# Optimization experiments

Measured on AMD Instinct MI355X. Metric: run time of the kernel, lower is better.

## Reference

```python
import jax, jax.numpy as jnp
import numpy as np

N_NODES = 100000
N_EDGES = 3200000
G_EDGES = 1600000
D_FEAT = 256
K_CLUSTERS = 16
COLLAPSE_REG = 0.1


def setup_inputs() -> dict:
    key = jax.random.key(0)
    ks = jax.random.split(key, 12)
    inp = {
        'features': jax.random.normal(ks[0], (N_NODES, D_FEAT), dtype=jnp.float32),
        'W': jax.random.normal(ks[1], (D_FEAT, K_CLUSTERS), dtype=jnp.float32) / np.sqrt(D_FEAT),
        'b': jnp.zeros((K_CLUSTERS,), dtype=jnp.float32),
        'adj_src': jax.random.randint(ks[2], (N_EDGES,), 0, N_NODES, dtype=jnp.int32),
        'adj_dst': jax.random.randint(ks[3], (N_EDGES,), 0, N_NODES, dtype=jnp.int32),
        'adj_val': jax.random.uniform(ks[4], (N_EDGES,), dtype=jnp.float32),
        'g1_src': jax.random.randint(ks[5], (G_EDGES,), 0, N_NODES, dtype=jnp.int32),
        'g1_dst': jax.random.randint(ks[6], (G_EDGES,), 0, N_NODES, dtype=jnp.int32),
        'g1_val': jax.random.uniform(ks[7], (G_EDGES,), dtype=jnp.float32),
        'g2_src': jax.random.randint(ks[8], (G_EDGES,), 0, N_NODES, dtype=jnp.int32),
        'g2_dst': jax.random.randint(ks[9], (G_EDGES,), 0, N_NODES, dtype=jnp.int32),
        'g2_val': jax.random.uniform(ks[10], (G_EDGES,), dtype=jnp.float32),
        'lamda': 1,
    }
    return inp


def _spmm(src, dst, val, X, n):
    # (sparse A) @ X where A[src, dst] = val : out[i] = sum_j A[i,j] X[j]
    return jax.ops.segment_sum(val[:, None] * X[dst], src, num_segments=n)


def _col_degrees(src, dst, val, n):
    # tf.sparse.reduce_sum(A, axis=0): column sums
    return jax.ops.segment_sum(val, dst, num_segments=n)


def reference(features, W, b, adj_src, adj_dst, adj_val,
              g1_src, g1_dst, g1_val, g2_src, g2_dst, g2_val, lamda):
    n = features.shape[0]
    k = W.shape[1]
    # soft cluster assignments  [n, k]
    S = jax.nn.softmax(features @ W + b, axis=1)
    cluster_sizes = jnp.sum(S, axis=0)            # [k]
    S_pool = S / cluster_sizes                    # [n, k]

    # full-graph modularity
    deg = _col_degrees(adj_src, adj_dst, adj_val, n)  # [n]
    m = jnp.sum(deg)                                  # total edge weight
    AS = _spmm(adj_src, adj_dst, adj_val, S, n)       # [n, k]
    graph_pooled = AS.T @ S                           # [k, k]
    dS = deg @ S                                      # [k] = S^T deg
    normalizer = jnp.outer(dS, dS) / 2.0 / m          # [k, k]
    spectral_loss = -jnp.trace(graph_pooled - normalizer) / 2.0 / m

    # per-group modularity Q_g
    def group_Q(src, dst, val):
        gdeg = _col_degrees(src, dst, val, n)
        gm = jnp.sum(gdeg)
        safe_gm = jnp.where(gm > 0, gm, 1.0)
        gAS = _spmm(src, dst, val, S, n)
        g_pooled = gAS.T @ S
        gdS = gdeg @ S
        g_norm = jnp.outer(gdS, gdS) / 2.0 / safe_gm
        Qg = jnp.trace(g_pooled - g_norm) / 2.0 / m
        return jnp.where(gm > 0, Qg, 0.0), gm

    Q1, m1 = group_Q(g1_src, g1_dst, g1_val)
    Q2, m2 = group_Q(g2_src, g2_dst, g2_val)
    Q_min = jnp.minimum(Q1, Q2)
    g_edges_mean = (m1 + m2) / 2.0
    edge_ratio = m / (g_edges_mean + 1e-8)
    fairness_loss = edge_ratio * (-Q_min)

    collapse_loss = (jnp.linalg.norm(cluster_sizes) / n) * jnp.sqrt(jnp.float32(k)) - 1.0

    total_loss = spectral_loss + lamda * fairness_loss + COLLAPSE_REG * collapse_loss

    features_pooled = jax.nn.selu(S_pool.T @ features)  # [k, d]
    return features_pooled, S, total_loss
```

## Files before the change

### kernel.cpp

```cpp
#include <hip/hip_runtime.h>
#include <cstddef>
#include <cstdint>


#define G1_MAX   1024
#define EGRID    2048
#define NSEG     16
#define OFF_E    0
#define SZ_E     (3 * 18 * EGRID)
#define OFF_R    (OFF_E + SZ_E)
#define OFF_G    (OFF_R + 4112)
#define OFF_F8   (OFF_G + 64)

#define TROWS    32
#define RPAD2    134

#define BLK0     1024
#define BLK12    512

typedef int      iv4 __attribute__((ext_vector_type(4)));
typedef float    fv4 __attribute__((ext_vector_type(4)));
typedef _Float16 hh;
typedef hh       h2  __attribute__((ext_vector_type(2)));

#if __has_builtin(__builtin_amdgcn_cvt_pk_f32_fp8)
#define HW_FP8 1
#endif

__device__ __forceinline__ h2 bch2(unsigned u) { return __builtin_bit_cast(h2, u); }

__device__ __forceinline__ float fdot2(h2 a, h2 b, float c)
{
#if __has_builtin(__builtin_amdgcn_fdot2)
    return __builtin_amdgcn_fdot2(a, b, c, false);
#else
    return fmaf((float)a[0], (float)b[0], fmaf((float)a[1], (float)b[1], c));
#endif
}

__device__ __forceinline__ h2 pk16(float x, float y)
{
#if __has_builtin(__builtin_amdgcn_cvt_pkrtz)
    return __builtin_bit_cast(h2, __builtin_amdgcn_cvt_pkrtz(x, y));
#else
    h2 r; r[0] = (hh)x; r[1] = (hh)y; return r;
#endif
}

__device__ __forceinline__ unsigned f32_to_e4m3(float f)
{
    unsigned bits = __float_as_uint(f);
    unsigned s = bits >> 31;
    int e32 = (int)((bits >> 23) & 255);
    unsigned m23 = bits & 0x7FFFFF;
    int e = e32 - 120;
    unsigned out;
    if (e32 == 0) out = 0;
    else if (e <= 0) {
        float av = fabsf(f);
        int q = (int)(av * 512.0f + 0.5f);
        out = (unsigned)q;
    } else if (e > 15) out = (15u << 3) | 6u;
    else {
        unsigned m3 = (m23 + 0x80000u) >> 20;
        if (m3 == 8u) { m3 = 0u; ++e; if (e > 15) { e = 15; m3 = 6u; } }
        out = ((unsigned)e << 3) | m3;
    }
    return out | (s << 7);
}

__device__ __forceinline__ void decode16(uint4 r, float* o, const float* lut)
{
#ifdef HW_FP8
    #pragma unroll
    for (int j = 0; j < 4; ++j) {
        unsigned u = (&r.x)[j];
        auto lo = __builtin_amdgcn_cvt_pk_f32_fp8(u, false);
        auto hi = __builtin_amdgcn_cvt_pk_f32_fp8(u, true);
        o[4*j]   = lo[0]; o[4*j+1] = lo[1];
        o[4*j+2] = hi[0]; o[4*j+3] = hi[1];
    }
#else
    #pragma unroll
    for (int j = 0; j < 4; ++j) {
        unsigned u = (&r.x)[j];
        #pragma unroll
        for (int q = 0; q < 4; ++q)
            o[4*j+q] = lut[(u >> (8*q)) & 255];
    }
#endif
}

__global__ void __launch_bounds__(256)
k_rows(const float* __restrict__ F, const float* __restrict__ W,
       const float* __restrict__ b, float* __restrict__ S_out,
       unsigned* __restrict__ S_f8, float* __restrict__ ws_P, int n, int n_tiles)
{
    __shared__ h2    Wt_h2[16][RPAD2];
    __shared__ h2    rows_h2[TROWS][RPAD2];
    __shared__ float S_lds[TROWS][17];
    __shared__ float cs_red[256];

    const int t = threadIdx.x;

    for (int idx = t; idx < 2048; idx += 256) {
        int k = idx & 15, p = idx >> 4;
        Wt_h2[k][p] = pk16(W[(2*p) * 16 + k], W[(2*p + 1) * 16 + k]);
    }

    const float bk = b[t & 15];
    const int rl = t >> 4;
    const int kl = t & 15;
    const int kp = t & 15;
    const int cp = t >> 4;

    h2 Pa[8];
    #pragma unroll
    for (int j = 0; j < 8; ++j) Pa[j] = pk16(0.f, 0.f);
    float cs_acc = 0.f;

    float4 stg[8];
    auto load_tile = [&](int tl) {
        const float4* F4 = (const float4*)(F + (size_t)tl * TROWS * 256);
        #pragma unroll
        for (int q = 0; q < 8; ++q) {
            int idx = t + (q << 8);
            int r = idx >> 6;
            float4 z = {0.f, 0.f, 0.f, 0.f};
            stg[q] = (tl * TROWS + r < n) ? F4[idx] : z;
        }
    };
    if (blockIdx.x < (unsigned)n_tiles) load_tile(blockIdx.x);
    __syncthreads();

    for (int tile = blockIdx.x; tile < n_tiles; tile += gridDim.x) {
        #pragma unroll
        for (int q = 0; q < 8; ++q) {
            int idx = t + (q << 8);
            int r = idx >> 6, c4 = idx & 63;
            rows_h2[r][c4 * 2]     = pk16(stg[q].x, stg[q].y);
            rows_h2[r][c4 * 2 + 1] = pk16(stg[q].z, stg[q].w);
        }
        __syncthreads();

        {
            int nt2 = tile + gridDim.x;
            if (nt2 < n_tiles) load_tile(nt2);
        }

        float a0 = 0.f, a1 = 0.f;
        #pragma unroll 8
        for (int dd = 0; dd < 32; ++dd) {
            uint4 wv = *(const uint4*)&Wt_h2[kl][dd << 2];
            uint4 r0 = *(const uint4*)&rows_h2[rl][dd << 2];
            uint4 r1 = *(const uint4*)&rows_h2[rl + 16][dd << 2];
            #pragma unroll
            for (int j = 0; j < 4; ++j) {
                h2 wj = bch2((&wv.x)[j]);
                a0 = fdot2(wj, bch2((&r0.x)[j]), a0);
                a1 = fdot2(wj, bch2((&r1.x)[j]), a1);
            }
        }
        a0 += bk; a1 += bk;

        float mx0 = a0, mx1 = a1;
        #pragma unroll
        for (int o = 8; o; o >>= 1) {
            mx0 = fmaxf(mx0, __shfl_xor(mx0, o, 16));
            mx1 = fmaxf(mx1, __shfl_xor(mx1, o, 16));
        }
        float e0 = __expf(a0 - mx0), e1 = __expf(a1 - mx1);
        float s0 = e0, s1 = e1;
        #pragma unroll
        for (int o = 8; o; o >>= 1) {
            s0 += __shfl_xor(s0, o, 16);
            s1 += __shfl_xor(s1, o, 16);
        }
        float sv0 = e0 / s0, sv1 = e1 / s1;

        const bool v0 = (tile * TROWS + rl) < n;
        const bool v1 = (tile * TROWS + rl + 16) < n;
        if (v0) { S_out[(((size_t)(tile * TROWS + rl)) << 4) + kl] = sv0; cs_acc += sv0; }
        if (v1) { S_out[(((size_t)(tile * TROWS + rl + 16)) << 4) + kl] = sv1; cs_acc += sv1; }
        S_lds[rl][kl]      = v0 ? sv0 : 0.f;
        S_lds[rl + 16][kl] = v1 ? sv1 : 0.f;
        __syncthreads();

        if (t < 128) {
            int r = t >> 2, c = t & 3;
            int row = tile * TROWS + r;
            if (row < n) {
                unsigned u = f32_to_e4m3(S_lds[r][4*c])
                           | (f32_to_e4m3(S_lds[r][4*c+1]) << 8)
                           | (f32_to_e4m3(S_lds[r][4*c+2]) << 16)
                           | (f32_to_e4m3(S_lds[r][4*c+3]) << 24);
                S_f8[((size_t)row << 2) + c] = u;
            }
        }

        #pragma unroll 4
        for (int r = 0; r < TROWS; ++r) {
            float sv = S_lds[r][kp];
            h2 svh = pk16(sv, sv);
            uint4 fa = *(const uint4*)&rows_h2[r][cp << 3];
            uint4 fb = *(const uint4*)&rows_h2[r][(cp << 3) + 4];
            #pragma unroll
            for (int j = 0; j < 4; ++j) {
                Pa[j]     = svh * bch2((&fa.x)[j]) + Pa[j];
                Pa[4 + j] = svh * bch2((&fb.x)[j]) + Pa[4 + j];
            }
        }
        __syncthreads();
    }

    {
        float o16[16];
        #pragma unroll
        for (int j = 0; j < 8; ++j) {
            o16[2*j]     = (float)Pa[j][0];
            o16[2*j + 1] = (float)Pa[j][1];
        }
        float* dst = ws_P + (size_t)blockIdx.x * 4112 + kp * 256 + (cp << 4);
        #pragma unroll
        for (int j = 0; j < 4; ++j)
            *(float4*)&dst[4*j] = make_float4(o16[4*j], o16[4*j+1], o16[4*j+2], o16[4*j+3]);
    }
    cs_red[t] = cs_acc;
    __syncthreads();
    if (t < 16) {
        float ssum = 0.f;
        #pragma unroll
        for (int i = 0; i < 16; ++i) ssum += cs_red[t + (i << 4)];
        ws_P[(size_t)blockIdx.x * 4112 + 4096 + t] = ssum;
    }
}

__global__ void __launch_bounds__(256)
k_reduce(const float* __restrict__ ws_P, float* __restrict__ ws_red, int nb)
{
    const int seg  = blockIdx.x & (NSEG - 1);
    const int jblk = blockIdx.x / NSEG;
    const int idx  = jblk * 256 + threadIdx.x;
    if (idx >= 4112) return;
    const int chunk = (nb + NSEG - 1) / NSEG;
    const int b0 = seg * chunk;
    const int b1 = min(nb, b0 + chunk);
    float s = 0.f;
    for (int bb = b0; bb < b1; ++bb)
        s += ws_P[(size_t)bb * 4112 + idx];
    atomicAdd(&ws_red[idx], s);
}

__global__ void __launch_bounds__(256, 4)
k_edge(const int* __restrict__ src0, const int* __restrict__ dst0,
       const float* __restrict__ val0, int n0,
       const int* __restrict__ src1, const int* __restrict__ dst1,
       const float* __restrict__ val1, int n1,
       const int* __restrict__ src2, const int* __restrict__ dst2,
       const float* __restrict__ val2, int n2,
       const uint4* __restrict__ S8, float* __restrict__ ws_e,
       int b0, int b1)
{
#ifndef HW_FP8
    __shared__ float lut[256];
    if (threadIdx.x < 256) {
        int i = threadIdx.x;
        int e_ = (i >> 3) & 15, m_ = i & 7, s_ = i >> 7;
        float v = e_ ? ldexpf((float)(8 + m_), e_ - 10) : ldexpf((float)m_, -9);
        lut[i] = s_ ? -v : v;
    }
    __syncthreads();
    const float* lutp = lut;
#else
    const float* lutp = nullptr;
#endif

    int g, bb, nblk, nE;
    const int* src; const int* dst; const float* val;
    if ((int)blockIdx.x < b0)      { g = 0; bb = blockIdx.x;      nblk = b0;             src = src0; dst = dst0; val = val0; nE = n0; }
    else if ((int)blockIdx.x < b1) { g = 1; bb = blockIdx.x - b0; nblk = b1 - b0;        src = src1; dst = dst1; val = val1; nE = n1; }
    else                           { g = 2; bb = blockIdx.x - b1; nblk = gridDim.x - b1; src = src2; dst = dst2; val = val2; nE = n2; }

    float m_acc = 0.f, tr_acc = 0.f;
    float gds[16];
    #pragma unroll
    for (int k = 0; k < 16; ++k) gds[k] = 0.f;

    const int nv = nE >> 2;
    const iv4* s4 = (const iv4*)src;
    const iv4* d4 = (const iv4*)dst;
    const fv4* v4 = (const fv4*)val;
    const int stride = nblk * 256;

    for (int i = bb * 256 + threadIdx.x; i < nv; i += stride) {
        iv4 sa = __builtin_nontemporal_load(&s4[i]);
        iv4 da = __builtin_nontemporal_load(&d4[i]);
        fv4 va = __builtin_nontemporal_load(&v4[i]);
        uint4 rs[4], rd[4];
        #pragma unroll
        for (int e = 0; e < 4; ++e) {
            rs[e] = S8[sa[e]];
            rd[e] = S8[da[e]];
        }
        #pragma unroll
        for (int e = 0; e < 4; ++e) {
            float sv[16], dv[16];
            decode16(rs[e], sv, lutp);
            decode16(rd[e], dv, lutp);
            float v = va[e];
            float dot = 0.f;
            #pragma unroll
            for (int k = 0; k < 16; ++k) dot = fmaf(sv[k], dv[k], dot);
            m_acc += v;
            tr_acc = fmaf(v, dot, tr_acc);
            #pragma unroll
            for (int k = 0; k < 16; ++k) gds[k] = fmaf(v, dv[k], gds[k]);
        }
    }

    if (bb == 0) {
        int e = (nv << 2) + threadIdx.x;
        if (e < nE) {
            float sv[16], dv[16];
            decode16(S8[src[e]], sv, lutp);
            decode16(S8[dst[e]], dv, lutp);
            float v = val[e];
            float dot = 0.f;
            #pragma unroll
            for (int k = 0; k < 16; ++k) dot = fmaf(sv[k], dv[k], dot);
            m_acc += v;
            tr_acc = fmaf(v, dot, tr_acc);
            #pragma unroll
            for (int k = 0; k < 16; ++k) gds[k] = fmaf(v, dv[k], gds[k]);
        }
    }

    #pragma unroll
    for (int o = 32; o; o >>= 1) {
        m_acc  += __shfl_xor(m_acc, o);
        tr_acc += __shfl_xor(tr_acc, o);
        #pragma unroll
        for (int k = 0; k < 16; ++k) gds[k] += __shfl_xor(gds[k], o);
    }
    __shared__ float wred[4][18];
    const int wid = threadIdx.x >> 6, lane = threadIdx.x & 63;
    if (lane == 0) {
        wred[wid][0] = m_acc; wred[wid][1] = tr_acc;
        #pragma unroll
        for (int k = 0; k < 16; ++k) wred[wid][2 + k] = gds[k];
    }
    __syncthreads();
    if (threadIdx.x < 18) {
        float s = wred[0][threadIdx.x] + wred[1][threadIdx.x]
                + wred[2][threadIdx.x] + wred[3][threadIdx.x];
        ws_e[(size_t)g * 18 * EGRID + (size_t)threadIdx.x * EGRID + bb] = s;
    }
}

__global__ void __launch_bounds__(256)
k_ereduce(const float* __restrict__ ws_e, float* __restrict__ G54,
          int g0, int g1, int g2)
{
    const int p = blockIdx.x;
    const int g = p / 18, slot = p % 18;
    int grids[3] = {g0, g1, g2};
    const int gb = grids[g];
    const float* base = ws_e + (size_t)g * 18 * EGRID + (size_t)slot * EGRID;

    const int t = threadIdx.x;
    float s = 0.f;
    for (int bb = t; bb < gb; bb += 256) s += base[bb];
    #pragma unroll
    for (int o = 32; o; o >>= 1) s += __shfl_xor(s, o);

    __shared__ float wr[4];
    if ((t & 63) == 0) wr[t >> 6] = s;
    __syncthreads();
    if (t == 0) G54[p] = wr[0] + wr[1] + wr[2] + wr[3];
}

__global__ void __launch_bounds__(256)
k_final(const float* __restrict__ ws_red, const float* __restrict__ G54,
        const void* __restrict__ lamda_ptr, float* __restrict__ out, int n)
{
    __shared__ float G[54];
    const int t = threadIdx.x;
    if (t < 54) G[t] = G54[t];
    __syncthreads();

    const float* P  = ws_red;
    const float* cs = ws_red + 4096;

    const float scale = 1.0507009873554805f;
    const float alpha = 1.6732632423543772f;
    for (int idx = t; idx < 4096; idx += 256) {
        int k = idx >> 8;
        float x = P[idx] / cs[k];
        float y = x > 0.f ? scale * x : scale * alpha * (expf(x) - 1.f);
        out[idx] = y;
    }

    if (t == 0) {
        int   li = *(const int*)lamda_ptr;
        float lf = *(const float*)lamda_ptr;
        float lamda = (li > -100000 && li < 100000) ? (float)li : lf;

        float m = G[0], trA = G[1];
        float ds2 = 0.f;
        for (int k = 0; k < 16; ++k) ds2 += G[2 + k] * G[2 + k];
        float spectral = -(trA - ds2 / (2.f * m)) / (2.f * m);

        float Q[2], gm[2];
        for (int g = 0; g < 2; ++g) {
            const float* Gg = G + 18 * (g + 1);
            float mg = Gg[0], trg = Gg[1];
            float gds2 = 0.f;
            for (int k = 0; k < 16; ++k) gds2 += Gg[2 + k] * Gg[2 + k];
            float safe = mg > 0.f ? mg : 1.f;
            float q = (trg - gds2 / (2.f * safe)) / (2.f * m);
            Q[g]  = mg > 0.f ? q : 0.f;
            gm[g] = mg;
        }
        float Qmin = fminf(Q[0], Q[1]);
        float gmean = 0.5f * (gm[0] + gm[1]);
        float fairness = (m / (gmean + 1e-8f)) * (-Qmin);

        float csn = 0.f;
        for (int k = 0; k < 16; ++k) csn += cs[k] * cs[k];
        float collapse = (sqrtf(csn) / (float)n) * 4.f - 1.f;

        out[4096 + (size_t)n * 16] = spectral + lamda * fairness + 0.1f * collapse;
    }
}

extern "C" void kernel_launch(void* const* d_in, const int* in_sizes, int n_in,
                              void* d_out, int out_size, void* d_ws, size_t ws_size,
                              hipStream_t stream)
{
    const float* F       = (const float*)d_in[0];
    const float* W       = (const float*)d_in[1];
    const float* b       = (const float*)d_in[2];
    const int*   adj_src = (const int*)d_in[3];
    const int*   adj_dst = (const int*)d_in[4];
    const float* adj_val = (const float*)d_in[5];
    const int*   g1_src  = (const int*)d_in[6];
    const int*   g1_dst  = (const int*)d_in[7];
    const float* g1_val  = (const float*)d_in[8];
    const int*   g2_src  = (const int*)d_in[9];
    const int*   g2_dst  = (const int*)d_in[10];
    const float* g2_val  = (const float*)d_in[11];
    const void*  lamda_p = d_in[12];

    const int n  = in_sizes[0] / 256;
    const int nE = in_sizes[3];
    const int n1 = in_sizes[6];
    const int n2 = in_sizes[9];

    float* out   = (float*)d_out;
    float* S_out = out + 4096;

    float* ws   = (float*)d_ws;
    float* ws_e = ws + OFF_E;
    float* ws_r = ws + OFF_R;
    float* ws_g = ws + OFF_G;
    unsigned* S8 = (unsigned*)(ws + OFF_F8);
    const size_t off_p = (size_t)OFF_F8 + (size_t)n * 4;
    float* ws_P = ws + off_p;

    const int n_tiles = (n + TROWS - 1) / TROWS;
    long avail = ((long)(ws_size / 4) - (long)off_p) / 4112;
    int grid1 = n_tiles < G1_MAX ? n_tiles : G1_MAX;
    if (avail < grid1) grid1 = (int)avail;
    if (grid1 < 1) grid1 = 1;

    (void)hipMemsetAsync(ws_r, 0, 4112 * sizeof(float), stream);

    k_rows<<<grid1, 256, 0, stream>>>(F, W, b, S_out, S8, ws_P, n, n_tiles);
    k_reduce<<<17 * NSEG, 256, 0, stream>>>(ws_P, ws_r, grid1);

    const int b0 = BLK0, b1g = BLK12, b2g = BLK12;
    k_edge<<<b0 + b1g + b2g, 256, 0, stream>>>(
        adj_src, adj_dst, adj_val, nE,
        g1_src, g1_dst, g1_val, n1,
        g2_src, g2_dst, g2_val, n2,
        (const uint4*)S8, ws_e, b0, b0 + b1g);

    k_ereduce<<<54, 256, 0, stream>>>(ws_e, ws_g, b0, b1g, b2g);
    k_final<<<1, 256, 0, stream>>>(ws_r, ws_g, lamda_p, out, n);
}
```

Baseline: 153.2 us.

## Use MFMA f16 instructions for softmax logits and pooled-feature accumulation in k_rows

Replaces the scalar fdot2 logits computation and the packed-half FMA accumulation of S^T·F with 16x16x32 f16 MFMA instructions. It adds a transposed LDS copy of each feature tile and a transposed f16 copy of S, and splits the K dimension across waves with an LDS reduction. S is now written from f16-rounded values, which lowers its precision. Accumulation is now in fp32 rather than fp16. The extra LDS transposes and syncs add overhead, but the compute-bound inner loops should shrink.

```diff
diff --git a/kernel.cpp b/kernel.cpp
--- a/kernel.cpp
+++ b/kernel.cpp
@@ -13,15 +13,19 @@
 #define OFF_F8   (OFF_G + 64)
 
 #define TROWS    32
-#define RPAD2    134
+#define RSTR     264
+#define TSTR     40
 
 #define BLK0     1024
 #define BLK12    512
 
-typedef int      iv4 __attribute__((ext_vector_type(4)));
-typedef float    fv4 __attribute__((ext_vector_type(4)));
+typedef int      iv4  __attribute__((ext_vector_type(4)));
+typedef float    fv4  __attribute__((ext_vector_type(4)));
+typedef unsigned uv4  __attribute__((ext_vector_type(4)));
 typedef _Float16 hh;
-typedef hh       h2  __attribute__((ext_vector_type(2)));
+typedef hh       h2   __attribute__((ext_vector_type(2)));
+typedef hh       h8   __attribute__((ext_vector_type(8)));
+typedef float    f32x4 __attribute__((ext_vector_type(4)));
 
 #if __has_builtin(__builtin_amdgcn_cvt_pk_f32_fp8)
 #define HW_FP8 1
@@ -29,22 +33,17 @@
 
 __device__ __forceinline__ h2 bch2(unsigned u) { return __builtin_bit_cast(h2, u); }
 
-__device__ __forceinline__ float fdot2(h2 a, h2 b, float c)
-{
-#if __has_builtin(__builtin_amdgcn_fdot2)
-    return __builtin_amdgcn_fdot2(a, b, c, false);
+__device__ __forceinline__ unsigned pk16u(float x, float y)
+{
+#if __has_builtin(__builtin_amdgcn_cvt_pkrtz)
+    return __builtin_bit_cast(unsigned, __builtin_amdgcn_cvt_pkrtz(x, y));
 #else
-    return fmaf((float)a[0], (float)b[0], fmaf((float)a[1], (float)b[1], c));
+    h2 r; r[0] = (hh)x; r[1] = (hh)y; return __builtin_bit_cast(unsigned, r);
 #endif
 }
-
-__device__ __forceinline__ h2 pk16(float x, float y)
-{
-#if __has_builtin(__builtin_amdgcn_cvt_pkrtz)
-    return __builtin_bit_cast(h2, __builtin_amdgcn_cvt_pkrtz(x, y));
-#else
-    h2 r; r[0] = (hh)x; r[1] = (hh)y; return r;
-#endif
+__device__ __forceinline__ unsigned short h16(float x)
+{
+    return (unsigned short)(pk16u(x, 0.f) & 0xFFFFu);
 }
 
 __device__ __forceinline__ unsigned f32_to_e4m3(float f)
@@ -96,27 +95,28 @@
        const float* __restrict__ b, float* __restrict__ S_out,
        unsigned* __restrict__ S_f8, float* __restrict__ ws_P, int n, int n_tiles)
 {
-    __shared__ h2    Wt_h2[16][RPAD2];
-    __shared__ h2    rows_h2[TROWS][RPAD2];
-    __shared__ float S_lds[TROWS][17];
+    __shared__ unsigned short Wt_u16[16][RSTR];
+    __shared__ unsigned short rows_u16[TROWS][RSTR];
+    __shared__ unsigned short rowsT_u16[256][TSTR];
+    __shared__ unsigned short St_u16[16][TSTR];
+    __shared__ float Sred[2][16][17];
     __shared__ float cs_red[256];
 
     const int t = threadIdx.x;
-
-    for (int idx = t; idx < 2048; idx += 256) {
-        int k = idx & 15, p = idx >> 4;
-        Wt_h2[k][p] = pk16(W[(2*p) * 16 + k], W[(2*p + 1) * 16 + k]);
-    }
-
-    const float bk = b[t & 15];
-    const int rl = t >> 4;
-    const int kl = t & 15;
-    const int kp = t & 15;
-    const int cp = t >> 4;
-
-    h2 Pa[8];
+    const int w = t >> 6;
+    const int l = t & 63;
+    const int l15 = l & 15;
+    const int lg  = l >> 4;
+
+    for (int idx = t; idx < 4096; idx += 256) {
+        int k = idx >> 4, nn = idx & 15;
+        Wt_u16[nn][k] = h16(W[idx]);
+    }
+    const float bk = b[l15];
+
+    f32x4 pacc[4];
     #pragma unroll
-    for (int j = 0; j < 8; ++j) Pa[j] = pk16(0.f, 0.f);
+    for (int j = 0; j < 4; ++j) pacc[j] = (f32x4){0.f, 0.f, 0.f, 0.f};
     float cs_acc = 0.f;
 
     float4 stg[8];
@@ -124,22 +124,26 @@
         const float4* F4 = (const float4*)(F + (size_t)tl * TROWS * 256);
         #pragma unroll
         for (int q = 0; q < 8; ++q) {
-            int idx = t + (q << 8);
-            int r = idx >> 6;
+            int r = (t >> 6) + 4 * q;
             float4 z = {0.f, 0.f, 0.f, 0.f};
-            stg[q] = (tl * TROWS + r < n) ? F4[idx] : z;
+            stg[q] = (tl * TROWS + r < n) ? F4[t + (q << 8)] : z;
         }
     };
     if (blockIdx.x < (unsigned)n_tiles) load_tile(blockIdx.x);
     __syncthreads();
 
     for (int tile = blockIdx.x; tile < n_tiles; tile += gridDim.x) {
+        const int c4 = t & 63;
         #pragma unroll
         for (int q = 0; q < 8; ++q) {
-            int idx = t + (q << 8);
-            int r = idx >> 6, c4 = idx & 63;
-            rows_h2[r][c4 * 2]     = pk16(stg[q].x, stg[q].y);
-            rows_h2[r][c4 * 2 + 1] = pk16(stg[q].z, stg[q].w);
+            int r = (t >> 6) + 4 * q;
+            unsigned u0 = pk16u(stg[q].x, stg[q].y);
+            unsigned u1 = pk16u(stg[q].z, stg[q].w);
+            *(uint2*)&rows_u16[r][c4 << 2] = make_uint2(u0, u1);
+            rowsT_u16[(c4 << 2) + 0][r] = (unsigned short)(u0 & 0xFFFFu);
+            rowsT_u16[(c4 << 2) + 1][r] = (unsigned short)(u0 >> 16);
+            rowsT_u16[(c4 << 2) + 2][r] = (unsigned short)(u1 & 0xFFFFu);
+            rowsT_u16[(c4 << 2) + 3][r] = (unsigned short)(u1 >> 16);
         }
         __syncthreads();
 
@@ -148,82 +152,94 @@
             if (nt2 < n_tiles) load_tile(nt2);
         }
 
-        float a0 = 0.f, a1 = 0.f;
-        #pragma unroll 8
-        for (int dd = 0; dd < 32; ++dd) {
-            uint4 wv = *(const uint4*)&Wt_h2[kl][dd << 2];
-            uint4 r0 = *(const uint4*)&rows_h2[rl][dd << 2];
-            uint4 r1 = *(const uint4*)&rows_h2[rl + 16][dd << 2];
-            #pragma unroll
-            for (int j = 0; j < 4; ++j) {
-                h2 wj = bch2((&wv.x)[j]);
-                a0 = fdot2(wj, bch2((&r0.x)[j]), a0);
-                a1 = fdot2(wj, bch2((&r1.x)[j]), a1);
+        const int mt  = w & 1;
+        const int ks0 = (w >> 1) * 4;
+        f32x4 c0 = (f32x4){0.f, 0.f, 0.f, 0.f};
+        #pragma unroll
+        for (int s = 0; s < 4; ++s) {
+            int k0 = (ks0 + s) << 5;
+            uv4 av = *(const uv4*)&rows_u16[(mt << 4) + l15][k0 + (lg << 3)];
+            uv4 bv = *(const uv4*)&Wt_u16[l15][k0 + (lg << 3)];
+            c0 = __builtin_amdgcn_mfma_f32_16x16x32_f16(
+                     __builtin_bit_cast(h8, av), __builtin_bit_cast(h8, bv),
+                     c0, 0, 0, 0);
+        }
+        if (w >= 2) {
+            #pragma unroll
+            for (int p = 0; p < 4; ++p)
+                Sred[mt][(lg << 2) + p][l15] = c0[p];
+        }
+        __syncthreads();
+
+        if (w < 2) {
+            float lv[4];
+            #pragma unroll
+            for (int p = 0; p < 4; ++p)
+                lv[p] = c0[p] + Sred[mt][(lg << 2) + p][l15] + bk;
+            float mx[4], sm[4];
+            #pragma unroll
+            for (int p = 0; p < 4; ++p) mx[p] = lv[p];
+            #pragma unroll
+            for (int o = 8; o; o >>= 1)
+                #pragma unroll
+                for (int p = 0; p < 4; ++p)
+                    mx[p] = fmaxf(mx[p], __shfl_xor(mx[p], o));
+            #pragma unroll
+            for (int p = 0; p < 4; ++p) { lv[p] = __expf(lv[p] - mx[p]); sm[p] = lv[p]; }
+            #pragma unroll
+            for (int o = 8; o; o >>= 1)
+                #pragma unroll
+                for (int p = 0; p < 4; ++p)
+                    sm[p] += __shfl_xor(sm[p], o);
+            float sv[4];
+            int rbase = tile * TROWS + (mt << 4) + (lg << 2);
+            #pragma unroll
+            for (int p = 0; p < 4; ++p) {
+                sv[p] = lv[p] / sm[p];
+                if (rbase + p < n) cs_acc += sv[p];
             }
-        }
-        a0 += bk; a1 += bk;
-
-        float mx0 = a0, mx1 = a1;
-        #pragma unroll
-        for (int o = 8; o; o >>= 1) {
-            mx0 = fmaxf(mx0, __shfl_xor(mx0, o, 16));
-            mx1 = fmaxf(mx1, __shfl_xor(mx1, o, 16));
-        }
-        float e0 = __expf(a0 - mx0), e1 = __expf(a1 - mx1);
-        float s0 = e0, s1 = e1;
-        #pragma unroll
-        for (int o = 8; o; o >>= 1) {
-            s0 += __shfl_xor(s0, o, 16);
-            s1 += __shfl_xor(s1, o, 16);
-        }
-        float sv0 = e0 / s0, sv1 = e1 / s1;
-
-        const bool v0 = (tile * TROWS + rl) < n;
-        const bool v1 = (tile * TROWS + rl + 16) < n;
-        if (v0) { S_out[(((size_t)(tile * TROWS + rl)) << 4) + kl] = sv0; cs_acc += sv0; }
-        if (v1) { S_out[(((size_t)(tile * TROWS + rl + 16)) << 4) + kl] = sv1; cs_acc += sv1; }
-        S_lds[rl][kl]      = v0 ? sv0 : 0.f;
-        S_lds[rl + 16][kl] = v1 ? sv1 : 0.f;
+            unsigned su0 = pk16u(sv[0], sv[1]);
+            unsigned su1 = pk16u(sv[2], sv[3]);
+            *(uint2*)&St_u16[l15][(mt << 4) + (lg << 2)] = make_uint2(su0, su1);
+        }
         __syncthreads();
 
         if (t < 128) {
             int r = t >> 2, c = t & 3;
             int row = tile * TROWS + r;
             if (row < n) {
-                unsigned u = f32_to_e4m3(S_lds[r][4*c])
-                           | (f32_to_e4m3(S_lds[r][4*c+1]) << 8)
-                           | (f32_to_e4m3(S_lds[r][4*c+2]) << 16)
-                           | (f32_to_e4m3(S_lds[r][4*c+3]) << 24);
+                float v0 = (float)__builtin_bit_cast(hh, St_u16[4*c + 0][r]);
+                float v1 = (float)__builtin_bit_cast(hh, St_u16[4*c + 1][r]);
+                float v2 = (float)__builtin_bit_cast(hh, St_u16[4*c + 2][r]);
+                float v3 = (float)__builtin_bit_cast(hh, St_u16[4*c + 3][r]);
+                *(float4*)&S_out[((size_t)row << 4) + 4*c] = make_float4(v0, v1, v2, v3);
+                unsigned u = f32_to_e4m3(v0) | (f32_to_e4m3(v1) << 8)
+                           | (f32_to_e4m3(v2) << 16) | (f32_to_e4m3(v3) << 24);
                 S_f8[((size_t)row << 2) + c] = u;
             }
         }
 
-        #pragma unroll 4
-        for (int r = 0; r < TROWS; ++r) {
-            float sv = S_lds[r][kp];
-            h2 svh = pk16(sv, sv);
-            uint4 fa = *(const uint4*)&rows_h2[r][cp << 3];
-            uint4 fb = *(const uint4*)&rows_h2[r][(cp << 3) + 4];
+        {
+            uv4 sa = *(const uv4*)&St_u16[l15][lg << 3];
+            h8  ah = __builtin_bit_cast(h8, sa);
             #pragma unroll
             for (int j = 0; j < 4; ++j) {
-                Pa[j]     = svh * bch2((&fa.x)[j]) + Pa[j];
-                Pa[4 + j] = svh * bch2((&fb.x)[j]) + Pa[4 + j];
+                int nc = (w << 2) + j;
+                uv4 bv = *(const uv4*)&rowsT_u16[(nc << 4) + l15][lg << 3];
+                pacc[j] = __builtin_amdgcn_mfma_f32_16x16x32_f16(
+                              ah, __builtin_bit_cast(h8, bv), pacc[j], 0, 0, 0);
             }
         }
         __syncthreads();
     }
 
     {
-        float o16[16];
-        #pragma unroll
-        for (int j = 0; j < 8; ++j) {
-            o16[2*j]     = (float)Pa[j][0];
-            o16[2*j + 1] = (float)Pa[j][1];
-        }
-        float* dst = ws_P + (size_t)blockIdx.x * 4112 + kp * 256 + (cp << 4);
+        float* dst = ws_P + (size_t)blockIdx.x * 4112;
         #pragma unroll
         for (int j = 0; j < 4; ++j)
-            *(float4*)&dst[4*j] = make_float4(o16[4*j], o16[4*j+1], o16[4*j+2], o16[4*j+3]);
+            #pragma unroll
+            for (int p = 0; p < 4; ++p)
+                dst[((lg << 2) + p) * 256 + (w << 6) + (j << 4) + l15] = pacc[j][p];
     }
     cs_red[t] = cs_acc;
     __syncthreads();
```

Measured after the change: 161.6 us. 1.05x slower.
